# Optimization experiments

Measured on AMD Instinct MI355X. Metric: run time of the kernel, lower is better.

Reference implementation:

```python
import jax, jax.numpy as jnp
import numpy as np

B, T, C = 8, 2048, 512
H = 8
DH = C // H
MLP = 4 * C
EPS = 1e-5


def _ln(x, w, b):
    m = jnp.mean(x, axis=-1, keepdims=True)
    v = jnp.mean(jnp.square(x - m), axis=-1, keepdims=True)
    return (x - m) * jax.lax.rsqrt(v + EPS) * w + b


def setup_inputs() -> dict:
    key = jax.random.key(0)
    ks = jax.random.split(key, 12)
    s = 0.02
    return {
        "x": jax.random.normal(ks[0], (B, T, C), jnp.float32),
        "c": jax.random.normal(ks[1], (B, C), jnp.float32),
        "qkv_w": jax.random.normal(ks[2], (3 * C, C), jnp.float32) * s,
        "qkv_b": jnp.zeros((3 * C,), jnp.float32),
        "proj_w": jax.random.normal(ks[3], (C, C), jnp.float32) * s,
        "proj_b": jnp.zeros((C,), jnp.float32),
        "ada_w": jax.random.normal(ks[4], (6 * C, C), jnp.float32) * s,
        "ada_b": jnp.zeros((6 * C,), jnp.float32),
        "fc1_w": jax.random.normal(ks[5], (MLP, C), jnp.float32) * s,
        "fc1_b": jnp.zeros((MLP,), jnp.float32),
        "fc2_w": jax.random.normal(ks[6], (C, MLP), jnp.float32) * s,
        "fc2_b": jnp.zeros((C,), jnp.float32),
        "ln1_w": jnp.ones((C,), jnp.float32),
        "ln1_b": jnp.zeros((C,), jnp.float32),
        "ln2_w": jnp.ones((C,), jnp.float32),
        "ln2_b": jnp.zeros((C,), jnp.float32),
    }


def reference(x, c, qkv_w, qkv_b, proj_w, proj_b, ada_w, ada_b,
              fc1_w, fc1_b, fc2_w, fc2_b, ln1_w, ln1_b, ln2_w, ln2_b):
    # AdaLN modulation: SiLU -> Linear -> chunk into 6 [B,C] pieces
    mod = jax.nn.silu(c) @ ada_w.T + ada_b  # [B, 6C]
    sh_msa, sc_msa, g_msa, sh_mlp, sc_mlp, g_mlp = jnp.split(mod, 6, axis=1)

    # --- attention branch ---
    h = _ln(x, ln1_w, ln1_b) * (1.0 + sc_msa[:, None, :]) + sh_msa[:, None, :]
    qkv = h @ qkv_w.T + qkv_b  # [B, T, 3C]
    q, k, v = jnp.split(qkv, 3, axis=-1)
    q = q.reshape(B, T, H, DH).transpose(0, 2, 1, 3)  # [B,H,T,Dh]
    k = k.reshape(B, T, H, DH).transpose(0, 2, 1, 3)
    v = v.reshape(B, T, H, DH).transpose(0, 2, 1, 3)
    scores = jnp.einsum('bhqd,bhkd->bhqk', q, k) * (1.0 / np.sqrt(DH))
    w = jax.nn.softmax(scores, axis=-1)
    o = jnp.einsum('bhqk,bhkd->bhqd', w, v)  # [B,H,T,Dh]
    o = o.transpose(0, 2, 1, 3).reshape(B, T, C)
    attn = o @ proj_w.T + proj_b
    x = x + g_msa[:, None, :] * attn

    # --- MLP branch ---
    h2 = _ln(x, ln2_w, ln2_b) * (1.0 + sc_mlp[:, None, :]) + sh_mlp[:, None, :]
    m = jax.nn.gelu(h2 @ fc1_w.T + fc1_b, approximate=True) @ fc2_w.T + fc2_b
    return x + g_mlp[:, None, :] * m
```

## Files before the change

kernel.cpp:

```cpp
#include <hip/hip_runtime.h>
#include <cstdint>
#include <cstddef>

typedef unsigned short u16;
typedef short v8s __attribute__((ext_vector_type(8)));
typedef short v4s __attribute__((ext_vector_type(4)));
typedef float v4f __attribute__((ext_vector_type(4)));
typedef float f32x16 __attribute__((ext_vector_type(16)));
typedef unsigned int v4u __attribute__((ext_vector_type(4)));
typedef unsigned short v4u16 __attribute__((ext_vector_type(4)));

#define TT 2048
#define CC 512

__device__ __forceinline__ u16 f2bf(float f) {
    unsigned u = __float_as_uint(f);
    u += 0x7fffu + ((u >> 16) & 1u);
    return (u16)(u >> 16);
}

__device__ __forceinline__ unsigned cvt_pk_bf16(float lo, float hi) {
    unsigned r;
    asm("v_cvt_pk_bf16_f32 %0, %1, %2" : "=v"(r) : "v"(lo), "v"(hi));
    return r;
}

__device__ __forceinline__ void swap32(unsigned a, unsigned b, unsigned& x, unsigned& y) {
#if __has_builtin(__builtin_amdgcn_permlane32_swap)
    auto r = __builtin_amdgcn_permlane32_swap(a, b, false, false);
    x = r[0]; y = r[1];
#else
    unsigned bx = (unsigned)__shfl_xor((int)b, 32, 64);
    unsigned ax = (unsigned)__shfl_xor((int)a, 32, 64);
    bool hi5 = (threadIdx.x & 32) != 0;
    x = hi5 ? bx : a;
    y = hi5 ? b : ax;
#endif
}

__device__ __forceinline__ void gl2lds16(const void* g, void* l) {
    __builtin_amdgcn_global_load_lds(
        (const __attribute__((address_space(1))) unsigned int*)g,
        (__attribute__((address_space(3))) unsigned int*)l,
        16, 0, 0);
}

__global__ __launch_bounds__(256) void f2bf_k(const float* __restrict__ s,
                                              u16* __restrict__ d, int n) {
    int i = (blockIdx.x * 256 + threadIdx.x) * 4;
    if (i >= n) return;
    float4 v = *(const float4*)(s + i);
    v4u16 r;
    r[0] = f2bf(v.x); r[1] = f2bf(v.y); r[2] = f2bf(v.z); r[3] = f2bf(v.w);
    *(v4u16*)(d + i) = r;
}

__global__ __launch_bounds__(256) void ada_kernel(const float* __restrict__ c,
                                                  const float* __restrict__ W,
                                                  const float* __restrict__ bias,
                                                  float* __restrict__ mod) {
    int idx = blockIdx.x * 4 + (threadIdx.x >> 6);
    int l = threadIdx.x & 63;
    int bb = idx / 3072;
    int n = idx - bb * 3072;
    const float* cp = c + bb * CC;
    const float* wp = W + (size_t)n * CC;
    float s = 0.f;
    #pragma unroll
    for (int i = 0; i < 8; ++i) {
        int k = l * 8 + i;
        float cv = cp[k];
        float sil = cv / (1.f + __expf(-cv));
        s += sil * wp[k];
    }
    #pragma unroll
    for (int off = 32; off; off >>= 1) s += __shfl_xor(s, off, 64);
    if (l == 0) mod[idx] = s + bias[n];
}

__global__ __launch_bounds__(256) void ln_mod_kernel(const float* __restrict__ X,
                                                     const float* __restrict__ lnw,
                                                     const float* __restrict__ lnb,
                                                     const float* __restrict__ mod,
                                                     int sh_off, int sc_off,
                                                     u16* __restrict__ out) {
    int row = blockIdx.x * 4 + (threadIdx.x >> 6);
    int l = threadIdx.x & 63;
    int b = row >> 11;
    const float* xr = X + (size_t)row * CC + l * 8;
    float4 va = *(const float4*)(xr);
    float4 vb = *(const float4*)(xr + 4);
    float v[8] = {va.x, va.y, va.z, va.w, vb.x, vb.y, vb.z, vb.w};
    float s = 0.f;
    #pragma unroll
    for (int i = 0; i < 8; ++i) s += v[i];
    #pragma unroll
    for (int off = 32; off; off >>= 1) s += __shfl_xor(s, off, 64);
    float mean = s * (1.f / CC);
    float q = 0.f;
    #pragma unroll
    for (int i = 0; i < 8; ++i) { float d = v[i] - mean; q += d * d; }
    #pragma unroll
    for (int off = 32; off; off >>= 1) q += __shfl_xor(q, off, 64);
    float rstd = rsqrtf(q * (1.f / CC) + 1e-5f);
    int col = l * 8;
    const float* shp = mod + b * 3072 + sh_off + col;
    const float* scp = mod + b * 3072 + sc_off + col;
    v8s st;
    #pragma unroll
    for (int i = 0; i < 8; ++i) {
        float hv = (v[i] - mean) * rstd * lnw[col + i] + lnb[col + i];
        float r = hv * (1.f + scp[i]) + shp[i];
        st[i] = (short)f2bf(r);
    }
    *(v8s*)(out + (size_t)row * CC + col) = st;
}

template <int MODE>
__global__ __launch_bounds__(256)
void gemm_bt(const u16* __restrict__ A, const u16* __restrict__ W,
             const float* __restrict__ bias, void* __restrict__ outp,
             const float* __restrict__ resid, const float* __restrict__ gate,
             int M, int N, int K) {
    __shared__ alignas(16) u16 Al[2][4096];
    __shared__ alignas(16) u16 Bl[2][4096];
    const int bn = blockIdx.x << 7, bm = blockIdx.y << 7;
    const int tid = threadIdx.x;
    const int w = tid >> 6, l = tid & 63;
    const int hi = l >> 4, lo = l & 15;
    const int wr = (w >> 1) << 6, wc = (w & 1) << 6;

    v4f acc[4][4] = {};

    const int srow = l >> 2;
    const int sp = l & 3;
    const int NT = K >> 5;

    auto stage = [&](int buf, int kt) {
        const int k0 = kt << 5;
        #pragma unroll
        for (int i = 0; i < 2; ++i) {
            const int c = w + (i << 2);
            const int row = (c << 4) + srow;
            const int lg = sp ^ ((row >> 1) & 3);
            gl2lds16(A + (size_t)(bm + row) * K + k0 + (lg << 3), &Al[buf][c << 9]);
            gl2lds16(W + (size_t)(bn + row) * K + k0 + (lg << 3), &Bl[buf][c << 9]);
        }
    };

    stage(0, 0);
    __syncthreads();
    int cur = 0;
    for (int t = 0; t < NT; ++t) {
        if (t + 1 < NT) stage(cur ^ 1, t + 1);
        const u16* Ab = Al[cur];
        const u16* Bb = Bl[cur];
        v8s aF[4], bF[4];
        #pragma unroll
        for (int mi = 0; mi < 4; ++mi) {
            int r = wr + (mi << 4) + lo;
            aF[mi] = *(const v8s*)(Ab + (r << 5) + ((hi ^ ((r >> 1) & 3)) << 3));
        }
        #pragma unroll
        for (int ni = 0; ni < 4; ++ni) {
            int r = wc + (ni << 4) + lo;
            bF[ni] = *(const v8s*)(Bb + (r << 5) + ((hi ^ ((r >> 1) & 3)) << 3));
        }
        #pragma unroll
        for (int mi = 0; mi < 4; ++mi)
            #pragma unroll
            for (int ni = 0; ni < 4; ++ni)
                acc[mi][ni] = __builtin_amdgcn_mfma_f32_16x16x32_bf16(
                    aF[mi], bF[ni], acc[mi][ni], 0, 0, 0);
        __syncthreads();
        cur ^= 1;
    }

    #pragma unroll
    for (int mi = 0; mi < 4; ++mi) {
        #pragma unroll
        for (int ni = 0; ni < 4; ++ni) {
            int col = bn + wc + (ni << 4) + lo;
            float bv = bias[col];
            #pragma unroll
            for (int j = 0; j < 4; ++j) {
                int row = bm + wr + (mi << 4) + hi * 4 + j;
                float v = acc[mi][ni][j] + bv;
                if constexpr (MODE == 0) {
                    ((u16*)outp)[(size_t)row * N + col] = f2bf(v);
                } else if constexpr (MODE == 1) {
                    float u2 = 1.5957691216057308f * (v + 0.044715f * v * v * v);
                    float g = v / (1.f + __expf(-u2));
                    ((u16*)outp)[(size_t)row * N + col] = f2bf(g);
                } else {
                    float r = resid[(size_t)row * N + col];
                    float gt = gate[(row >> 11) * 3072 + col];
                    ((float*)outp)[(size_t)row * N + col] = r + gt * v;
                }
            }
        }
    }
}

__global__ __launch_bounds__(512, 1)
void attn_kernel(const u16* __restrict__ qkv, u16* __restrict__ O) {
    __shared__ alignas(16) u16 smem[18432];
    const int tid = threadIdx.x;
    const int w = tid >> 6, l = tid & 63;
    const int l31 = l & 31, l5 = l >> 5;
    const int bh = blockIdx.y, b = bh >> 3, h = bh & 7;
    const int qt = blockIdx.x;
    const float SC = 0.125f;

    const int qrow = qt * 256 + w * 32 + l31;
    const u16* qp = qkv + (size_t)(b * TT + qrow) * 1536 + h * 64;
    v8s qf[4];
    #pragma unroll
    for (int ks = 0; ks < 4; ++ks) qf[ks] = *(const v8s*)(qp + ks * 16 + l5 * 8);

    const int krow = (w << 3) + (l >> 3);
    const int kc = (l & 7) ^ (l >> 3);
    const int vp = tid >> 4;
    const int c4 = (tid & 15) << 2;

    auto stageK = [&](int kt, int buf) {
        gl2lds16(qkv + (size_t)(b * TT + kt * 64 + krow) * 1536 + 512 + h * 64 + kc * 8,
                 smem + buf * 4096 + (w << 9));
    };
    v4s va, vb;
    auto loadV = [&](int kt) {
        const u16* vs = qkv + (size_t)(b * TT + kt * 64 + 2 * vp) * 1536 + 1024 + h * 64 + c4;
        va = *(const v4s*)vs;
        vb = *(const v4s*)(vs + 1536);
    };
    auto writeV = [&](int buf) {
        char* Vb = (char*)(smem + 8192 + buf * 4096);
        #pragma unroll
        for (int e = 0; e < 4; ++e) {
            int d = c4 + e;
            unsigned pk = (unsigned)(u16)va[e] | ((unsigned)(u16)vb[e] << 16);
            *(unsigned*)(Vb + ((d << 7) | ((vp << 2) ^ ((d & 7) << 4)))) = pk;
        }
    };
    const int physbase = l31 & 7;
    auto afrag = [&](const char* base, int t, int ks) -> v8s {
        int row = t * 32 + l31;
        int phys = ((ks << 1) + l5) ^ physbase;
        return *(const v8s*)(base + (row << 7) + (phys << 4));
    };

    stageK(0, 0);
    loadV(0);
    writeV(0);
    __syncthreads();

    f32x16 st[2];
    f32x16 o[2] = {};
    float mrun = -1e30f, lrun = 0.f;
    int cur = 0;

    for (int kt = 0; kt < 32; ++kt) {
        if (kt + 1 < 32) { stageK(kt + 1, cur ^ 1); loadV(kt + 1); }
        const char* Kb = (const char*)(smem + cur * 4096);
        const char* Vb = (const char*)(smem + 8192 + cur * 4096);

        st[0] = (f32x16)0.f; st[1] = (f32x16)0.f;
        __builtin_amdgcn_s_setprio(1);
        #pragma unroll
        for (int ks = 0; ks < 4; ++ks) {
            v8s k0 = afrag(Kb, 0, ks);
            v8s k1 = afrag(Kb, 1, ks);
            st[0] = __builtin_amdgcn_mfma_f32_32x32x16_bf16(k0, qf[ks], st[0], 0, 0, 0);
            st[1] = __builtin_amdgcn_mfma_f32_32x32x16_bf16(k1, qf[ks], st[1], 0, 0, 0);
        }
        __builtin_amdgcn_s_setprio(0);

        float tmax = st[0][0];
        #pragma unroll
        for (int r = 1; r < 16; ++r) tmax = fmaxf(tmax, st[0][r]);
        #pragma unroll
        for (int r = 0; r < 16; ++r) tmax = fmaxf(tmax, st[1][r]);
        tmax = fmaxf(tmax, __shfl_xor(tmax, 32, 64));
        float mnew = fmaxf(mrun, tmax);
        float alpha = __expf((mrun - mnew) * SC);
        float rsum = 0.f;
        #pragma unroll
        for (int t2 = 0; t2 < 2; ++t2)
            #pragma unroll
            for (int r = 0; r < 16; ++r) {
                float p = __expf((st[t2][r] - mnew) * SC);
                st[t2][r] = p;
                rsum += p;
            }
        rsum += __shfl_xor(rsum, 32, 64);
        lrun = lrun * alpha + rsum;
        mrun = mnew;
        #pragma unroll
        for (int t2 = 0; t2 < 2; ++t2)
            #pragma unroll
            for (int r = 0; r < 16; ++r) o[t2][r] *= alpha;

        __builtin_amdgcn_s_setprio(1);
        #pragma unroll
        for (int ks = 0; ks < 4; ++ks) {
            const int tt = ks >> 1, rb = (ks & 1) * 8;
            unsigned pkA = cvt_pk_bf16(st[tt][rb + 0], st[tt][rb + 1]);
            unsigned pkB = cvt_pk_bf16(st[tt][rb + 4], st[tt][rb + 5]);
            unsigned pkC = cvt_pk_bf16(st[tt][rb + 2], st[tt][rb + 3]);
            unsigned pkD = cvt_pk_bf16(st[tt][rb + 6], st[tt][rb + 7]);
            unsigned w0, w1, w2, w3;
            swap32(pkA, pkB, w0, w2);
            swap32(pkC, pkD, w1, w3);
            v4u pw; pw[0] = w0; pw[1] = w1; pw[2] = w2; pw[3] = w3;
            v8s pa = __builtin_bit_cast(v8s, pw);
            v8s vf0 = afrag(Vb, 0, ks);
            v8s vf1 = afrag(Vb, 1, ks);
            o[0] = __builtin_amdgcn_mfma_f32_32x32x16_bf16(vf0, pa, o[0], 0, 0, 0);
            o[1] = __builtin_amdgcn_mfma_f32_32x32x16_bf16(vf1, pa, o[1], 0, 0, 0);
        }
        __builtin_amdgcn_s_setprio(0);

        if (kt + 1 < 32) writeV(cur ^ 1);
        __syncthreads();
        cur ^= 1;
    }

    float inv = 1.f / lrun;
    char* outw = (char*)smem + w * 4608;
    #pragma unroll
    for (int t2 = 0; t2 < 2; ++t2)
        #pragma unroll
        for (int r = 0; r < 16; r += 2) {
            int dh = t2 * 32 + (r & 3) + ((r >> 2) << 3) + (l5 << 2);
            unsigned pk = cvt_pk_bf16(o[t2][r] * inv, o[t2][r + 1] * inv);
            *(unsigned*)(outw + l31 * 144 + dh * 2) = pk;
        }
    __syncthreads();
    #pragma unroll
    for (int i = 0; i < 4; ++i) {
        int idx = (i << 9) + tid;
        int qq = idx >> 3, cch = idx & 7;
        v8s vd = *(const v8s*)((char*)smem + (qq >> 5) * 4608 + (qq & 31) * 144 + cch * 16);
        *(v8s*)(O + (size_t)(b * TT + qt * 256 + qq) * 512 + h * 64 + cch * 8) = vd;
    }
}

extern "C" void kernel_launch(void* const* d_in, const int* in_sizes, int n_in,
                              void* d_out, int out_size, void* d_ws, size_t ws_size,
                              hipStream_t stream) {
    const float* x = (const float*)d_in[0];
    const float* c = (const float*)d_in[1];
    const float* qkv_w = (const float*)d_in[2];
    const float* qkv_b = (const float*)d_in[3];
    const float* proj_w = (const float*)d_in[4];
    const float* proj_b = (const float*)d_in[5];
    const float* ada_w = (const float*)d_in[6];
    const float* ada_b = (const float*)d_in[7];
    const float* fc1_w = (const float*)d_in[8];
    const float* fc1_b = (const float*)d_in[9];
    const float* fc2_w = (const float*)d_in[10];
    const float* fc2_b = (const float*)d_in[11];
    const float* ln1_w = (const float*)d_in[12];
    const float* ln1_b = (const float*)d_in[13];
    const float* ln2_w = (const float*)d_in[14];
    const float* ln2_b = (const float*)d_in[15];

    char* p = (char*)d_ws;
    auto carve = [&](size_t bytes) -> char* {
        char* r = p;
        p += (bytes + 255) & ~(size_t)255;
        return r;
    };
    float* mod  = (float*)carve((size_t)8 * 3072 * 4);
    u16* hbuf   = (u16*)carve((size_t)16384 * 512 * 2);
    u16* qkvb   = (u16*)carve((size_t)16384 * 1536 * 2);
    u16* attno  = (u16*)carve((size_t)16384 * 512 * 2);
    float* x1   = (float*)carve((size_t)16384 * 512 * 4);
    u16* wq     = (u16*)carve((size_t)1536 * 512 * 2);
    u16* wpj    = (u16*)carve((size_t)512 * 512 * 2);
    u16* w1     = (u16*)carve((size_t)2048 * 512 * 2);
    u16* w2     = (u16*)carve((size_t)512 * 2048 * 2);
    u16* fc1g   = qkvb;

    f2bf_k<<<(1536 * 512) / 1024, 256, 0, stream>>>(qkv_w, wq, 1536 * 512);
    f2bf_k<<<(512 * 512) / 1024, 256, 0, stream>>>(proj_w, wpj, 512 * 512);
    f2bf_k<<<(2048 * 512) / 1024, 256, 0, stream>>>(fc1_w, w1, 2048 * 512);
    f2bf_k<<<(512 * 2048) / 1024, 256, 0, stream>>>(fc2_w, w2, 512 * 2048);

    ada_kernel<<<24576 / 4, 256, 0, stream>>>(c, ada_w, ada_b, mod);

    ln_mod_kernel<<<16384 / 4, 256, 0, stream>>>(x, ln1_w, ln1_b, mod, 0, 512, hbuf);
    gemm_bt<0><<<dim3(12, 128), 256, 0, stream>>>(hbuf, wq, qkv_b, qkvb,
                                                  nullptr, nullptr, 16384, 1536, 512);
    attn_kernel<<<dim3(8, 64), 512, 0, stream>>>(qkvb, attno);
    gemm_bt<2><<<dim3(4, 128), 256, 0, stream>>>(attno, wpj, proj_b, x1,
                                                 x, mod + 2 * 512, 16384, 512, 512);

    ln_mod_kernel<<<16384 / 4, 256, 0, stream>>>(x1, ln2_w, ln2_b, mod, 3 * 512, 4 * 512, hbuf);
    gemm_bt<1><<<dim3(16, 128), 256, 0, stream>>>(hbuf, w1, fc1_b, fc1g,
                                                  nullptr, nullptr, 16384, 2048, 512);
    gemm_bt<2><<<dim3(4, 128), 256, 0, stream>>>(fc1g, w2, fc2_b, (float*)d_out,
                                                 x1, mod + 5 * 512, 16384, 512, 2048);
}
```

Baseline: 321.0 us.

## Shrink attention blocks, add lazy softmax rescale, and XCD-swizzle GEMM grids

The attention kernel goes from 512-thread blocks covering 256 queries to 256-thread blocks covering 128 queries, with launch bounds asking for four blocks per CU. The grid becomes 1D and ordered so that a head's query tiles are spread out. Softmax now uses exp2 with a fused scale and only rescales the running output when the max grows by more than a threshold, which removes most per-tile multiplies. V staging is rewritten to load 8 rows per lane and write transposed 16-byte chunks. The GEMMs use a 1D grid remapped so consecutive tiles land on the same XCD for better L2 reuse. The lazy rescale keeps fp32 values bounded but could in principle allow larger intermediate sums.

```diff
diff --git a/kernel.cpp b/kernel.cpp
--- a/kernel.cpp
+++ b/kernel.cpp
@@ -4,7 +4,6 @@
 
 typedef unsigned short u16;
 typedef short v8s __attribute__((ext_vector_type(8)));
-typedef short v4s __attribute__((ext_vector_type(4)));
 typedef float v4f __attribute__((ext_vector_type(4)));
 typedef float f32x16 __attribute__((ext_vector_type(16)));
 typedef unsigned int v4u __attribute__((ext_vector_type(4)));
@@ -121,10 +120,13 @@
 void gemm_bt(const u16* __restrict__ A, const u16* __restrict__ W,
              const float* __restrict__ bias, void* __restrict__ outp,
              const float* __restrict__ resid, const float* __restrict__ gate,
-             int M, int N, int K) {
+             int NX, int N, int K) {
     __shared__ alignas(16) u16 Al[2][4096];
     __shared__ alignas(16) u16 Bl[2][4096];
-    const int bn = blockIdx.x << 7, bm = blockIdx.y << 7;
+    const int id = blockIdx.x;
+    const int wg = (id & 7) * (gridDim.x >> 3) + (id >> 3);
+    const int by = wg / NX, bx = wg - by * NX;
+    const int bn = bx << 7, bm = by << 7;
     const int tid = threadIdx.x;
     const int w = tid >> 6, l = tid & 63;
     const int hi = l >> 4, lo = l & 15;
@@ -202,46 +204,59 @@
     }
 }
 
-__global__ __launch_bounds__(512, 1)
+__global__ __launch_bounds__(256, 4)
 void attn_kernel(const u16* __restrict__ qkv, u16* __restrict__ O) {
-    __shared__ alignas(16) u16 smem[18432];
+    __shared__ alignas(16) u16 smem[16384];
     const int tid = threadIdx.x;
     const int w = tid >> 6, l = tid & 63;
     const int l31 = l & 31, l5 = l >> 5;
-    const int bh = blockIdx.y, b = bh >> 3, h = bh & 7;
-    const int qt = blockIdx.x;
-    const float SC = 0.125f;
-
-    const int qrow = qt * 256 + w * 32 + l31;
+    const int id = blockIdx.x;
+    const int bh = id & 63, b = bh >> 3, h = bh & 7;
+    const int qt = id >> 6;
+    const float SCL2 = 0.125f * 1.4426950408889634f;
+
+    const int qrow = qt * 128 + w * 32 + l31;
     const u16* qp = qkv + (size_t)(b * TT + qrow) * 1536 + h * 64;
     v8s qf[4];
     #pragma unroll
     for (int ks = 0; ks < 4; ++ks) qf[ks] = *(const v8s*)(qp + ks * 16 + l5 * 8);
 
-    const int krow = (w << 3) + (l >> 3);
-    const int kc = (l & 7) ^ (l >> 3);
-    const int vp = tid >> 4;
-    const int c4 = (tid & 15) << 2;
-
+    const int kr8 = l >> 3;
+    const int kc = (l & 7) ^ kr8;
     auto stageK = [&](int kt, int buf) {
-        gl2lds16(qkv + (size_t)(b * TT + kt * 64 + krow) * 1536 + 512 + h * 64 + kc * 8,
-                 smem + buf * 4096 + (w << 9));
-    };
-    v4s va, vb;
+        #pragma unroll
+        for (int i = 0; i < 2; ++i) {
+            int c = 2 * w + i;
+            gl2lds16(qkv + (size_t)(b * TT + kt * 64 + c * 8 + kr8) * 1536 + 512 + h * 64 + kc * 8,
+                     smem + buf * 4096 + c * 512);
+        }
+    };
+
+    const int d2 = l & 31;
+    const int oct = (2 * w + l5) & 7;
+    unsigned V2[8];
     auto loadV = [&](int kt) {
-        const u16* vs = qkv + (size_t)(b * TT + kt * 64 + 2 * vp) * 1536 + 1024 + h * 64 + c4;
-        va = *(const v4s*)vs;
-        vb = *(const v4s*)(vs + 1536);
+        const u16* vs = qkv + (size_t)(b * TT + kt * 64 + oct * 8) * 1536 + 1024 + h * 64 + 2 * d2;
+        #pragma unroll
+        for (int e = 0; e < 8; ++e)
+            V2[e] = *(const unsigned*)(vs + (size_t)e * 1536);
     };
     auto writeV = [&](int buf) {
-        char* Vb = (char*)(smem + 8192 + buf * 4096);
-        #pragma unroll
-        for (int e = 0; e < 4; ++e) {
-            int d = c4 + e;
-            unsigned pk = (unsigned)(u16)va[e] | ((unsigned)(u16)vb[e] << 16);
-            *(unsigned*)(Vb + ((d << 7) | ((vp << 2) ^ ((d & 7) << 4)))) = pk;
-        }
-    };
+        char* Vb = (char*)smem + 16384 + buf * 8192;
+        #pragma unroll
+        for (int p = 0; p < 2; ++p) {
+            int d = 2 * d2 + p;
+            v4u wv;
+            #pragma unroll
+            for (int i = 0; i < 4; ++i) {
+                unsigned a = V2[2 * i], bb2 = V2[2 * i + 1];
+                wv[i] = p ? ((a >> 16) | (bb2 & 0xffff0000u))
+                          : ((a & 0xffffu) | (bb2 << 16));
+            }
+            *(v4u*)(Vb + ((d << 7) | ((oct ^ (d & 7)) << 4))) = wv;
+        }
+    };
+
     const int physbase = l31 & 7;
     auto afrag = [&](const char* base, int t, int ks) -> v8s {
         int row = t * 32 + l31;
@@ -261,8 +276,8 @@
 
     for (int kt = 0; kt < 32; ++kt) {
         if (kt + 1 < 32) { stageK(kt + 1, cur ^ 1); loadV(kt + 1); }
-        const char* Kb = (const char*)(smem + cur * 4096);
-        const char* Vb = (const char*)(smem + 8192 + cur * 4096);
+        const char* Kb = (const char*)smem + cur * 8192;
+        const char* Vb = (const char*)smem + 16384 + cur * 8192;
 
         st[0] = (f32x16)0.f; st[1] = (f32x16)0.f;
         __builtin_amdgcn_s_setprio(1);
@@ -275,30 +290,38 @@
         }
         __builtin_amdgcn_s_setprio(0);
 
-        float tmax = st[0][0];
-        #pragma unroll
-        for (int r = 1; r < 16; ++r) tmax = fmaxf(tmax, st[0][r]);
-        #pragma unroll
-        for (int r = 0; r < 16; ++r) tmax = fmaxf(tmax, st[1][r]);
+        float tmax = fmaxf(fmaxf(st[0][0], st[0][1]), fmaxf(st[0][2], st[0][3]));
+        #pragma unroll
+        for (int r = 4; r < 16; r += 4)
+            tmax = fmaxf(tmax, fmaxf(fmaxf(st[0][r], st[0][r + 1]),
+                                     fmaxf(st[0][r + 2], st[0][r + 3])));
+        #pragma unroll
+        for (int r = 0; r < 16; r += 4)
+            tmax = fmaxf(tmax, fmaxf(fmaxf(st[1][r], st[1][r + 1]),
+                                     fmaxf(st[1][r + 2], st[1][r + 3])));
         tmax = fmaxf(tmax, __shfl_xor(tmax, 32, 64));
-        float mnew = fmaxf(mrun, tmax);
-        float alpha = __expf((mrun - mnew) * SC);
+        if (!__all(tmax - mrun <= 64.f)) {
+            float mnew = fmaxf(mrun, tmax);
+            float alpha = __builtin_exp2f((mrun - mnew) * SCL2);
+            #pragma unroll
+            for (int t2 = 0; t2 < 2; ++t2)
+                #pragma unroll
+                for (int r = 0; r < 16; ++r) o[t2][r] *= alpha;
+            lrun *= alpha;
+            mrun = mnew;
+        }
+        float msc = mrun * SCL2;
         float rsum = 0.f;
         #pragma unroll
         for (int t2 = 0; t2 < 2; ++t2)
             #pragma unroll
             for (int r = 0; r < 16; ++r) {
-                float p = __expf((st[t2][r] - mnew) * SC);
+                float p = __builtin_exp2f(__builtin_fmaf(st[t2][r], SCL2, -msc));
                 st[t2][r] = p;
                 rsum += p;
             }
         rsum += __shfl_xor(rsum, 32, 64);
-        lrun = lrun * alpha + rsum;
-        mrun = mnew;
-        #pragma unroll
-        for (int t2 = 0; t2 < 2; ++t2)
-            #pragma unroll
-            for (int r = 0; r < 16; ++r) o[t2][r] *= alpha;
+        lrun += rsum;
 
         __builtin_amdgcn_s_setprio(1);
         #pragma unroll
@@ -338,10 +361,10 @@
     __syncthreads();
     #pragma unroll
     for (int i = 0; i < 4; ++i) {
-        int idx = (i << 9) + tid;
+        int idx = (i << 8) + tid;
         int qq = idx >> 3, cch = idx & 7;
         v8s vd = *(const v8s*)((char*)smem + (qq >> 5) * 4608 + (qq & 31) * 144 + cch * 16);
-        *(v8s*)(O + (size_t)(b * TT + qt * 256 + qq) * 512 + h * 64 + cch * 8) = vd;
+        *(v8s*)(O + (size_t)(b * TT + qt * 128 + qq) * 512 + h * 64 + cch * 8) = vd;
     }
 }
 
@@ -390,15 +413,15 @@
     ada_kernel<<<24576 / 4, 256, 0, stream>>>(c, ada_w, ada_b, mod);
 
     ln_mod_kernel<<<16384 / 4, 256, 0, stream>>>(x, ln1_w, ln1_b, mod, 0, 512, hbuf);
-    gemm_bt<0><<<dim3(12, 128), 256, 0, stream>>>(hbuf, wq, qkv_b, qkvb,
-                                                  nullptr, nullptr, 16384, 1536, 512);
-    attn_kernel<<<dim3(8, 64), 512, 0, stream>>>(qkvb, attno);
-    gemm_bt<2><<<dim3(4, 128), 256, 0, stream>>>(attno, wpj, proj_b, x1,
-                                                 x, mod + 2 * 512, 16384, 512, 512);
+    gemm_bt<0><<<12 * 128, 256, 0, stream>>>(hbuf, wq, qkv_b, qkvb,
+                                             nullptr, nullptr, 12, 1536, 512);
+    attn_kernel<<<1024, 256, 0, stream>>>(qkvb, attno);
+    gemm_bt<2><<<4 * 128, 256, 0, stream>>>(attno, wpj, proj_b, x1,
+                                            x, mod + 2 * 512, 4, 512, 512);
 
     ln_mod_kernel<<<16384 / 4, 256, 0, stream>>>(x1, ln2_w, ln2_b, mod, 3 * 512, 4 * 512, hbuf);
-    gemm_bt<1><<<dim3(16, 128), 256, 0, stream>>>(hbuf, w1, fc1_b, fc1g,
-                                                  nullptr, nullptr, 16384, 2048, 512);
-    gemm_bt<2><<<dim3(4, 128), 256, 0, stream>>>(fc1g, w2, fc2_b, (float*)d_out,
-                                                 x1, mod + 5 * 512, 16384, 512, 2048);
-}
+    gemm_bt<1><<<16 * 128, 256, 0, stream>>>(hbuf, w1, fc1_b, fc1g,
+                                             nullptr, nullptr, 16, 2048, 512);
+    gemm_bt<2><<<4 * 128, 256, 0, stream>>>(fc1g, w2, fc2_b, (float*)d_out,
+                                            x1, mod + 5 * 512, 4, 512, 2048);
+}
```

After: 322.3 us. Within noise of the previous version (+0.4%).
